# Kernel tuning notes

Hardware: AMD Instinct MI355X
Metric: run time of the kernel (lower is better)

## Reference

```python
import jax, jax.numpy as jnp
import numpy as np

TOP_K = 2

def setup_inputs() -> dict:
    key = jax.random.key(0)
    ks = jax.random.split(key, 5)
    B, S, H, F, E = 4, 512, 1024, 3584, 8
    x = jax.random.normal(ks[0], (B, S, H), dtype=jnp.float32)
    gate_w = jax.random.normal(ks[1], (H, E), dtype=jnp.float32) * (1.0 / np.sqrt(H))
    w1 = jax.random.normal(ks[2], (E, F, H), dtype=jnp.float32) * (1.0 / np.sqrt(H))
    w3 = jax.random.normal(ks[3], (E, F, H), dtype=jnp.float32) * (1.0 / np.sqrt(H))
    w2 = jax.random.normal(ks[4], (E, H, F), dtype=jnp.float32) * (1.0 / np.sqrt(F))
    return {"x": x, "gate_w": gate_w, "w1": w1, "w3": w3, "w2": w2}


def reference(x, gate_w, w1, w3, w2):
    # MoE top-2 routing (Mixtral-style), dense-dispatch formulation.
    B, S, H = x.shape
    E = gate_w.shape[1]
    xt = x.reshape(-1, H)                      # [T, H] flattened tokens
    T = xt.shape[0]
    logits = xt @ gate_w                       # [T, E] gate logits
    top_w, top_i = jax.lax.top_k(logits, TOP_K)    # [T, K]
    top_w = jax.nn.softmax(top_w, axis=-1)         # softmax over selected-k logits
    # combine[t, e] = routing weight of expert e for token t (0 if not selected)
    combine = jnp.zeros((T, E), dtype=xt.dtype)
    combine = combine.at[jnp.arange(T)[:, None], top_i].add(top_w)
    # SwiGLU experts: y_e = w2_e @ (silu(w1_e x) * (w3_e x))
    h = jnp.einsum('th,efh->tef', xt, w1)      # [T, E, F]
    g = jnp.einsum('th,efh->tef', xt, w3)      # [T, E, F]
    act = jax.nn.silu(h) * g                   # [T, E, F]
    out_e = jnp.einsum('tef,ehf->teh', act, w2)  # [T, E, H]
    out = jnp.einsum('teh,te->th', out_e, combine)  # weighted combine over experts
    return out.reshape(B, S, H)
```

## Files before the change

### kernel.cpp

```cpp
#include <hip/hip_runtime.h>
#include <hip/hip_bf16.h>
#include <stdint.h>

#define TOKENS 2048
#define HDIM 1024
#define FDIM 3584
#define NEXP 8
#define BK 32

typedef __attribute__((ext_vector_type(8))) short short8;
typedef __attribute__((ext_vector_type(4))) float floatx4;

#define AS1 __attribute__((address_space(1)))
#define AS3 __attribute__((address_space(3)))

__device__ __forceinline__ void glds16(const void* g, void* l) {
  __builtin_amdgcn_global_load_lds((const AS1 void*)g, (AS3 void*)l, 16, 0, 0);
}

__device__ __forceinline__ unsigned short f2bf(float f) {
  union { float f; unsigned int u; } c; c.f = f;
  unsigned int u = c.u;
  u += 0x7fffu + ((u >> 16) & 1u);
  return (unsigned short)(u >> 16);
}

__device__ __forceinline__ unsigned int pk2bf(float a, float b) {
  __hip_bfloat162 h = __float22bfloat162_rn(make_float2(a, b));
  union { __hip_bfloat162 h; unsigned int u; } c; c.h = h;
  return c.u;
}

__device__ __forceinline__ short8 pack_bf16(float4 c0, float4 c1) {
  union { short8 s; uint4 u; } o;
  o.u.x = pk2bf(c0.x, c0.y); o.u.y = pk2bf(c0.z, c0.w);
  o.u.z = pk2bf(c1.x, c1.y); o.u.w = pk2bf(c1.z, c1.w);
  return o.s;
}

__global__ void gate_kernel(const float* __restrict__ x,
                            const float* __restrict__ gw,
                            int* __restrict__ top_e,
                            float* __restrict__ top_w,
                            int* __restrict__ count) {
  int wv = threadIdx.x >> 6;
  int lane = threadIdx.x & 63;
  int t = blockIdx.x * 4 + wv;
  if (t >= TOKENS) return;
  float p[NEXP];
#pragma unroll
  for (int e = 0; e < NEXP; e++) p[e] = 0.f;
  const float* xr = x + (size_t)t * HDIM;
  for (int h = lane; h < HDIM; h += 64) {
    float xv = xr[h];
    const float4* g4 = (const float4*)(gw + (size_t)h * NEXP);
    float4 a = g4[0], b = g4[1];
    p[0] += xv * a.x; p[1] += xv * a.y; p[2] += xv * a.z; p[3] += xv * a.w;
    p[4] += xv * b.x; p[5] += xv * b.y; p[6] += xv * b.z; p[7] += xv * b.w;
  }
#pragma unroll
  for (int e = 0; e < NEXP; e++) {
#pragma unroll
    for (int off = 32; off > 0; off >>= 1) p[e] += __shfl_xor(p[e], off, 64);
  }
  if (lane == 0) {
    int i0 = 0;
    for (int e = 1; e < NEXP; e++) if (p[e] > p[i0]) i0 = e;
    int i1 = (i0 == 0) ? 1 : 0;
    for (int e = 0; e < NEXP; e++) if (e != i0 && p[e] > p[i1]) i1 = e;
    float l0 = p[i0], l1 = p[i1];
    float e1 = __expf(l1 - l0);
    float s = 1.f + e1;
    top_e[t * 2] = i0; top_e[t * 2 + 1] = i1;
    top_w[t * 2] = 1.f / s; top_w[t * 2 + 1] = e1 / s;
    atomicAdd(&count[i0], 1);
    atomicAdd(&count[i1], 1);
  }
}

__global__ void offsets_kernel(const int* __restrict__ count,
                               int* __restrict__ offs,
                               int* __restrict__ cursor) {
  if (threadIdx.x == 0 && blockIdx.x == 0) {
    int o = 0;
    for (int e = 0; e < NEXP; e++) { offs[e] = o; cursor[e] = o; o += count[e]; }
  }
}

__global__ void scatter_kernel(const int* __restrict__ top_e,
                               int* __restrict__ cursor,
                               int* __restrict__ tok_of,
                               int* __restrict__ slot_of) {
  int t = blockIdx.x * blockDim.x + threadIdx.x;
  if (t >= TOKENS) return;
#pragma unroll
  for (int k = 0; k < 2; k++) {
    int e = top_e[t * 2 + k];
    int g = atomicAdd(&cursor[e], 1);
    tok_of[g] = t;
    slot_of[t * 2 + k] = g;
  }
}

__global__ void xconv_kernel(const float* __restrict__ x,
                             unsigned short* __restrict__ xbf) {
  int i = (blockIdx.x * blockDim.x + threadIdx.x) * 4;
  float4 v = *(const float4*)(x + i);
  uint2 pk;
  pk.x = pk2bf(v.x, v.y);
  pk.y = pk2bf(v.z, v.w);
  *(uint2*)(xbf + i) = pk;
}

#define G1_BM 128
#define G1_BF 64

__global__ __launch_bounds__(256, 3)
void gemm1_kernel(const unsigned short* __restrict__ xbf,
                  const float* __restrict__ w1,
                  const float* __restrict__ w3,
                  const int* __restrict__ count,
                  const int* __restrict__ offs,
                  const int* __restrict__ tok_of,
                  unsigned short* __restrict__ act) {
  int e = blockIdx.z;
  int cnt = count[e];
  int m0 = blockIdx.y * G1_BM;
  if (m0 >= cnt) return;
  int f0 = blockIdx.x * G1_BF;
  int off_e = offs[e];

  __shared__ __align__(16) unsigned short sA[G1_BM * 32];
  __shared__ __align__(16) float sB1[G1_BF * 32];
  __shared__ __align__(16) float sB3[G1_BF * 32];

  int tid = threadIdx.x;
  int lane = tid & 63, wv = tid >> 6;

  const unsigned short* ag[2];
  char* alb[2];
  const float* g1p[2]; const float* g3p[2];
  char* blb[2];
#pragma unroll
  for (int p = 0; p < 2; p++) {
    int c = tid + p * 256;
    {
      int row = c >> 2, slot = c & 3;
      int gch = slot ^ ((row >> 1) & 3);
      int r = m0 + row;
      int tok = tok_of[off_e + (r < cnt ? r : 0)];
      ag[p] = xbf + (size_t)tok * HDIM + gch * 8;
      alb[p] = (char*)sA + (wv * 64 + p * 256) * 16;
    }
    {
      int row = c >> 3, slot = c & 7;
      int gch = slot ^ (row & 7);
      g1p[p] = w1 + ((size_t)e * FDIM + f0 + row) * HDIM + gch * 4;
      g3p[p] = w3 + ((size_t)e * FDIM + f0 + row) * HDIM + gch * 4;
      blb[p] = (char*)sB1 + (wv * 64 + p * 256) * 16;
    }
  }
  size_t b3delta = (char*)sB3 - (char*)sB1;

  int lrow = lane & 15, quad = lane >> 4;
  int wm = wv >> 1, wn = wv & 1;

  floatx4 acc1[4][2], acc3[4][2];
#pragma unroll
  for (int i = 0; i < 4; i++)
#pragma unroll
    for (int j = 0; j < 2; j++) {
      acc1[i][j] = (floatx4){0.f, 0.f, 0.f, 0.f};
      acc3[i][j] = (floatx4){0.f, 0.f, 0.f, 0.f};
    }

  for (int k0 = 0; k0 < HDIM; k0 += BK) {
    __syncthreads();
#pragma unroll
    for (int p = 0; p < 2; p++) {
      glds16(ag[p] + k0, alb[p]);
      glds16(g1p[p] + k0, blb[p]);
      glds16(g3p[p] + k0, blb[p] + b3delta);
    }
    __syncthreads();

    short8 af[4], b1f[2], b3f[2];
#pragma unroll
    for (int ms = 0; ms < 4; ms++) {
      int r = wm * 64 + ms * 16 + lrow;
      int sl = quad ^ ((r >> 1) & 3);
      af[ms] = *(const short8*)(sA + r * 32 + sl * 8);
    }
#pragma unroll
    for (int ns = 0; ns < 2; ns++) {
      int r = wn * 32 + ns * 16 + lrow;
      int s0 = (2 * quad) ^ (r & 7), s1 = (2 * quad + 1) ^ (r & 7);
      float4 c0 = *(const float4*)(sB1 + r * 32 + s0 * 4);
      float4 c1 = *(const float4*)(sB1 + r * 32 + s1 * 4);
      b1f[ns] = pack_bf16(c0, c1);
      float4 d0 = *(const float4*)(sB3 + r * 32 + s0 * 4);
      float4 d1 = *(const float4*)(sB3 + r * 32 + s1 * 4);
      b3f[ns] = pack_bf16(d0, d1);
    }
#pragma unroll
    for (int ms = 0; ms < 4; ms++)
#pragma unroll
      for (int ns = 0; ns < 2; ns++) {
        acc1[ms][ns] = __builtin_amdgcn_mfma_f32_16x16x32_bf16(af[ms], b1f[ns], acc1[ms][ns], 0, 0, 0);
        acc3[ms][ns] = __builtin_amdgcn_mfma_f32_16x16x32_bf16(af[ms], b3f[ns], acc3[ms][ns], 0, 0, 0);
      }
  }

#pragma unroll
  for (int ms = 0; ms < 4; ms++) {
#pragma unroll
    for (int reg = 0; reg < 4; reg++) {
      int slot = m0 + wm * 64 + ms * 16 + quad * 4 + reg;
      if (slot < cnt) {
        unsigned short* ar = act + (size_t)(off_e + slot) * FDIM + f0 + wn * 32;
#pragma unroll
        for (int ns = 0; ns < 2; ns++) {
          float h = acc1[ms][ns][reg];
          float g = acc3[ms][ns][reg];
          float a = h / (1.f + __expf(-h)) * g;
          ar[ns * 16 + lrow] = f2bf(a);
        }
      }
    }
  }
}

#define G2_BM 128
#define G2_BN 128
#define SPLITK 4
#define G2_KS (FDIM / SPLITK)

__global__ __launch_bounds__(256, 3)
void gemm2_kernel(const unsigned short* __restrict__ act,
                  const float* __restrict__ w2,
                  const int* __restrict__ count,
                  const int* __restrict__ offs,
                  float* __restrict__ part) {
  int zz = blockIdx.z;
  int e = zz & 7, sk = zz >> 3;
  int cnt = count[e];
  int m0 = blockIdx.y * G2_BM;
  if (m0 >= cnt) return;
  int h0 = blockIdx.x * G2_BN;
  int off_e = offs[e];
  int kb = sk * G2_KS;

  __shared__ __align__(16) unsigned short sA[G2_BM * 32];
  __shared__ __align__(16) float sB[G2_BN * 32];

  int tid = threadIdx.x;
  int lane = tid & 63, wv = tid >> 6;

  const unsigned short* ag[2];
  char* alb[2];
#pragma unroll
  for (int p = 0; p < 2; p++) {
    int c = tid + p * 256;
    int row = c >> 2, slot = c & 3;
    int gch = slot ^ ((row >> 1) & 3);
    int r = m0 + row;
    int rr = (r < cnt ? r : 0);
    ag[p] = act + (size_t)(off_e + rr) * FDIM + kb + gch * 8;
    alb[p] = (char*)sA + (wv * 64 + p * 256) * 16;
  }
  const float* bg[4];
  char* blb[4];
#pragma unroll
  for (int p = 0; p < 4; p++) {
    int c = tid + p * 256;
    int row = c >> 3, slot = c & 7;
    int gch = slot ^ (row & 7);
    bg[p] = w2 + ((size_t)e * HDIM + h0 + row) * FDIM + kb + gch * 4;
    blb[p] = (char*)sB + (wv * 64 + p * 256) * 16;
  }

  int lrow = lane & 15, quad = lane >> 4;
  int wm = wv >> 1, wn = wv & 1;

  floatx4 acc[4][4];
#pragma unroll
  for (int i = 0; i < 4; i++)
#pragma unroll
    for (int j = 0; j < 4; j++) acc[i][j] = (floatx4){0.f, 0.f, 0.f, 0.f};

  for (int k0 = 0; k0 < G2_KS; k0 += BK) {
    __syncthreads();
#pragma unroll
    for (int p = 0; p < 2; p++) glds16(ag[p] + k0, alb[p]);
#pragma unroll
    for (int p = 0; p < 4; p++) glds16(bg[p] + k0, blb[p]);
    __syncthreads();

    short8 af[4], bf[4];
#pragma unroll
    for (int ms = 0; ms < 4; ms++) {
      int r = wm * 64 + ms * 16 + lrow;
      int sl = quad ^ ((r >> 1) & 3);
      af[ms] = *(const short8*)(sA + r * 32 + sl * 8);
    }
#pragma unroll
    for (int ns = 0; ns < 4; ns++) {
      int r = wn * 64 + ns * 16 + lrow;
      int s0 = (2 * quad) ^ (r & 7), s1 = (2 * quad + 1) ^ (r & 7);
      float4 c0 = *(const float4*)(sB + r * 32 + s0 * 4);
      float4 c1 = *(const float4*)(sB + r * 32 + s1 * 4);
      bf[ns] = pack_bf16(c0, c1);
    }
#pragma unroll
    for (int ms = 0; ms < 4; ms++)
#pragma unroll
      for (int ns = 0; ns < 4; ns++)
        acc[ms][ns] = __builtin_amdgcn_mfma_f32_16x16x32_bf16(af[ms], bf[ns], acc[ms][ns], 0, 0, 0);
  }

#pragma unroll
  for (int ms = 0; ms < 4; ms++) {
#pragma unroll
    for (int reg = 0; reg < 4; reg++) {
      int slot = m0 + wm * 64 + ms * 16 + quad * 4 + reg;
      if (slot < cnt) {
        float* crow = part + ((size_t)sk * 4096 + off_e + slot) * HDIM + h0 + wn * 64;
#pragma unroll
        for (int ns = 0; ns < 4; ns++)
          crow[ns * 16 + lrow] = acc[ms][ns][reg];
      }
    }
  }
}

__global__ void combine_kernel(const float* __restrict__ part,
                               const int* __restrict__ slot_of,
                               const float* __restrict__ top_w,
                               float* __restrict__ out) {
  int t = blockIdx.x;
  int g0 = slot_of[t * 2], g1 = slot_of[t * 2 + 1];
  float w0 = top_w[t * 2], w1 = top_w[t * 2 + 1];
  int i = threadIdx.x;
  float4 s0 = {0.f, 0.f, 0.f, 0.f}, s1 = {0.f, 0.f, 0.f, 0.f};
#pragma unroll
  for (int sk = 0; sk < SPLITK; sk++) {
    float4 a = ((const float4*)(part + ((size_t)sk * 4096 + g0) * HDIM))[i];
    float4 b = ((const float4*)(part + ((size_t)sk * 4096 + g1) * HDIM))[i];
    s0.x += a.x; s0.y += a.y; s0.z += a.z; s0.w += a.w;
    s1.x += b.x; s1.y += b.y; s1.z += b.z; s1.w += b.w;
  }
  float4 r;
  r.x = w0 * s0.x + w1 * s1.x;
  r.y = w0 * s0.y + w1 * s1.y;
  r.z = w0 * s0.z + w1 * s1.z;
  r.w = w0 * s0.w + w1 * s1.w;
  ((float4*)(out + (size_t)t * HDIM))[i] = r;
}

extern "C" void kernel_launch(void* const* d_in, const int* in_sizes, int n_in,
                              void* d_out, int out_size, void* d_ws, size_t ws_size,
                              hipStream_t stream) {
  const float* x  = (const float*)d_in[0];
  const float* gw = (const float*)d_in[1];
  const float* w1 = (const float*)d_in[2];
  const float* w3 = (const float*)d_in[3];
  const float* w2 = (const float*)d_in[4];
  float* out = (float*)d_out;

  char* ws = (char*)d_ws;
  const size_t XBF_OFF = 0;
  const size_t ACT_OFF = 4ull << 20;
  const size_t PART_OFF = 36ull << 20;
  const size_t SML_OFF = 100ull << 20;

  unsigned short* xbf = (unsigned short*)(ws + XBF_OFF);
  unsigned short* act = (unsigned short*)(ws + ACT_OFF);
  float* part = (float*)(ws + PART_OFF);
  float* top_w = (float*)(ws + SML_OFF);
  int* top_e   = (int*)(ws + SML_OFF + 16384);
  int* slot_of = (int*)(ws + SML_OFF + 32768);
  int* tok_of  = (int*)(ws + SML_OFF + 49152);
  int* count   = (int*)(ws + SML_OFF + 65536);
  int* offs    = (int*)(ws + SML_OFF + 65536 + 32);
  int* cursor  = (int*)(ws + SML_OFF + 65536 + 64);

  hipMemsetAsync(count, 0, 96, stream);

  gate_kernel<<<TOKENS / 4, 256, 0, stream>>>(x, gw, top_e, top_w, count);
  offsets_kernel<<<1, 64, 0, stream>>>(count, offs, cursor);
  scatter_kernel<<<TOKENS / 256, 256, 0, stream>>>(top_e, cursor, tok_of, slot_of);
  xconv_kernel<<<(TOKENS * HDIM) / (256 * 4), 256, 0, stream>>>(x, xbf);
  gemm1_kernel<<<dim3(FDIM / G1_BF, TOKENS / G1_BM, NEXP), 256, 0, stream>>>(
      xbf, w1, w3, count, offs, tok_of, act);
  gemm2_kernel<<<dim3(HDIM / G2_BN, TOKENS / G2_BM, NEXP * SPLITK), 256, 0, stream>>>(
      act, w2, count, offs, part);
  combine_kernel<<<TOKENS, 256, 0, stream>>>(part, slot_of, top_w, out);
}
```

Before: 562.8 us.

## Pre-convert expert weights to bf16 and merge routing kernels into one

A new kernel converts w1, w3 and w2 from fp32 to bf16 in workspace on every call. Both GEMMs then stream bf16 weights straight into LDS, which halves weight bytes per tile and removes the per-iteration fp32→bf16 packing in the inner loop. This trades an extra full pass over the weights (fp32 read plus bf16 write) against the repeated fp32 weight traffic across M tiles. Separately, the histogram, offsets and scatter steps are fused into one single-block route kernel using shared-memory atomics, which removes the memset and two launches.

```diff
diff --git a/kernel.cpp b/kernel.cpp
--- a/kernel.cpp
+++ b/kernel.cpp
@@ -31,18 +31,10 @@
   return c.u;
 }
 
-__device__ __forceinline__ short8 pack_bf16(float4 c0, float4 c1) {
-  union { short8 s; uint4 u; } o;
-  o.u.x = pk2bf(c0.x, c0.y); o.u.y = pk2bf(c0.z, c0.w);
-  o.u.z = pk2bf(c1.x, c1.y); o.u.w = pk2bf(c1.z, c1.w);
-  return o.s;
-}
-
 __global__ void gate_kernel(const float* __restrict__ x,
                             const float* __restrict__ gw,
                             int* __restrict__ top_e,
-                            float* __restrict__ top_w,
-                            int* __restrict__ count) {
+                            float* __restrict__ top_w) {
   int wv = threadIdx.x >> 6;
   int lane = threadIdx.x & 63;
   int t = blockIdx.x * 4 + wv;
@@ -73,32 +65,40 @@
     float s = 1.f + e1;
     top_e[t * 2] = i0; top_e[t * 2 + 1] = i1;
     top_w[t * 2] = 1.f / s; top_w[t * 2 + 1] = e1 / s;
-    atomicAdd(&count[i0], 1);
-    atomicAdd(&count[i1], 1);
-  }
-}
-
-__global__ void offsets_kernel(const int* __restrict__ count,
-                               int* __restrict__ offs,
-                               int* __restrict__ cursor) {
-  if (threadIdx.x == 0 && blockIdx.x == 0) {
+  }
+}
+
+__global__ void route_kernel(const int* __restrict__ top_e,
+                             int* __restrict__ count,
+                             int* __restrict__ offs,
+                             int* __restrict__ tok_of,
+                             int* __restrict__ slot_of) {
+  __shared__ int hist[NEXP];
+  __shared__ int cur[NEXP];
+  int tid = threadIdx.x;
+  if (tid < NEXP) hist[tid] = 0;
+  __syncthreads();
+  int e[4];
+#pragma unroll
+  for (int j = 0; j < 4; j++) {
+    int i = tid * 4 + j;
+    e[j] = top_e[i];
+    atomicAdd(&hist[e[j]], 1);
+  }
+  __syncthreads();
+  if (tid == 0) {
     int o = 0;
-    for (int e = 0; e < NEXP; e++) { offs[e] = o; cursor[e] = o; o += count[e]; }
-  }
-}
-
-__global__ void scatter_kernel(const int* __restrict__ top_e,
-                               int* __restrict__ cursor,
-                               int* __restrict__ tok_of,
-                               int* __restrict__ slot_of) {
-  int t = blockIdx.x * blockDim.x + threadIdx.x;
-  if (t >= TOKENS) return;
-#pragma unroll
-  for (int k = 0; k < 2; k++) {
-    int e = top_e[t * 2 + k];
-    int g = atomicAdd(&cursor[e], 1);
-    tok_of[g] = t;
-    slot_of[t * 2 + k] = g;
+    for (int k = 0; k < NEXP; k++) {
+      offs[k] = o; cur[k] = o; count[k] = hist[k]; o += hist[k];
+    }
+  }
+  __syncthreads();
+#pragma unroll
+  for (int j = 0; j < 4; j++) {
+    int i = tid * 4 + j;
+    int g = atomicAdd(&cur[e[j]], 1);
+    tok_of[g] = i >> 1;
+    slot_of[i] = g;
   }
 }
 
@@ -112,13 +112,31 @@
   *(uint2*)(xbf + i) = pk;
 }
 
+__global__ void wconv_kernel(const float* __restrict__ w1,
+                             const float* __restrict__ w3,
+                             const float* __restrict__ w2,
+                             unsigned short* __restrict__ b1,
+                             unsigned short* __restrict__ b3,
+                             unsigned short* __restrict__ b2) {
+  int z = blockIdx.y;
+  const float* src = (z == 0) ? w1 : (z == 1) ? w3 : w2;
+  unsigned short* dst = (z == 0) ? b1 : (z == 1) ? b3 : b2;
+  size_t i = ((size_t)blockIdx.x * 256 + threadIdx.x) * 8;
+  float4 a = *(const float4*)(src + i);
+  float4 b = *(const float4*)(src + i + 4);
+  uint4 o;
+  o.x = pk2bf(a.x, a.y); o.y = pk2bf(a.z, a.w);
+  o.z = pk2bf(b.x, b.y); o.w = pk2bf(b.z, b.w);
+  *(uint4*)(dst + i) = o;
+}
+
 #define G1_BM 128
 #define G1_BF 64
 
 __global__ __launch_bounds__(256, 3)
 void gemm1_kernel(const unsigned short* __restrict__ xbf,
-                  const float* __restrict__ w1,
-                  const float* __restrict__ w3,
+                  const unsigned short* __restrict__ w1b,
+                  const unsigned short* __restrict__ w3b,
                   const int* __restrict__ count,
                   const int* __restrict__ offs,
                   const int* __restrict__ tok_of,
@@ -131,36 +149,35 @@
   int off_e = offs[e];
 
   __shared__ __align__(16) unsigned short sA[G1_BM * 32];
-  __shared__ __align__(16) float sB1[G1_BF * 32];
-  __shared__ __align__(16) float sB3[G1_BF * 32];
+  __shared__ __align__(16) unsigned short sB1[G1_BF * 32];
+  __shared__ __align__(16) unsigned short sB3[G1_BF * 32];
 
   int tid = threadIdx.x;
   int lane = tid & 63, wv = tid >> 6;
 
   const unsigned short* ag[2];
   char* alb[2];
-  const float* g1p[2]; const float* g3p[2];
-  char* blb[2];
 #pragma unroll
   for (int p = 0; p < 2; p++) {
     int c = tid + p * 256;
-    {
-      int row = c >> 2, slot = c & 3;
-      int gch = slot ^ ((row >> 1) & 3);
-      int r = m0 + row;
-      int tok = tok_of[off_e + (r < cnt ? r : 0)];
-      ag[p] = xbf + (size_t)tok * HDIM + gch * 8;
-      alb[p] = (char*)sA + (wv * 64 + p * 256) * 16;
-    }
-    {
-      int row = c >> 3, slot = c & 7;
-      int gch = slot ^ (row & 7);
-      g1p[p] = w1 + ((size_t)e * FDIM + f0 + row) * HDIM + gch * 4;
-      g3p[p] = w3 + ((size_t)e * FDIM + f0 + row) * HDIM + gch * 4;
-      blb[p] = (char*)sB1 + (wv * 64 + p * 256) * 16;
-    }
-  }
-  size_t b3delta = (char*)sB3 - (char*)sB1;
+    int row = c >> 2, slot = c & 3;
+    int gch = slot ^ ((row >> 1) & 3);
+    int r = m0 + row;
+    int tok = tok_of[off_e + (r < cnt ? r : 0)];
+    ag[p] = xbf + (size_t)tok * HDIM + gch * 8;
+    alb[p] = (char*)sA + (wv * 64 + p * 256) * 16;
+  }
+  const unsigned short *b1g, *b3g;
+  char *b1l, *b3l;
+  {
+    int row = tid >> 2, slot = tid & 3;
+    int gch = slot ^ ((row >> 1) & 3);
+    size_t wrow = (size_t)e * FDIM + f0 + row;
+    b1g = w1b + wrow * HDIM + gch * 8;
+    b3g = w3b + wrow * HDIM + gch * 8;
+    b1l = (char*)sB1 + (wv * 64) * 16;
+    b3l = (char*)sB3 + (wv * 64) * 16;
+  }
 
   int lrow = lane & 15, quad = lane >> 4;
   int wm = wv >> 1, wn = wv & 1;
@@ -177,11 +194,9 @@
   for (int k0 = 0; k0 < HDIM; k0 += BK) {
     __syncthreads();
 #pragma unroll
-    for (int p = 0; p < 2; p++) {
-      glds16(ag[p] + k0, alb[p]);
-      glds16(g1p[p] + k0, blb[p]);
-      glds16(g3p[p] + k0, blb[p] + b3delta);
-    }
+    for (int p = 0; p < 2; p++) glds16(ag[p] + k0, alb[p]);
+    glds16(b1g + k0, b1l);
+    glds16(b3g + k0, b3l);
     __syncthreads();
 
     short8 af[4], b1f[2], b3f[2];
@@ -194,13 +209,9 @@
 #pragma unroll
     for (int ns = 0; ns < 2; ns++) {
       int r = wn * 32 + ns * 16 + lrow;
-      int s0 = (2 * quad) ^ (r & 7), s1 = (2 * quad + 1) ^ (r & 7);
-      float4 c0 = *(const float4*)(sB1 + r * 32 + s0 * 4);
-      float4 c1 = *(const float4*)(sB1 + r * 32 + s1 * 4);
-      b1f[ns] = pack_bf16(c0, c1);
-      float4 d0 = *(const float4*)(sB3 + r * 32 + s0 * 4);
-      float4 d1 = *(const float4*)(sB3 + r * 32 + s1 * 4);
-      b3f[ns] = pack_bf16(d0, d1);
+      int sl = quad ^ ((r >> 1) & 3);
+      b1f[ns] = *(const short8*)(sB1 + r * 32 + sl * 8);
+      b3f[ns] = *(const short8*)(sB3 + r * 32 + sl * 8);
     }
 #pragma unroll
     for (int ms = 0; ms < 4; ms++)
@@ -237,7 +248,7 @@
 
 __global__ __launch_bounds__(256, 3)
 void gemm2_kernel(const unsigned short* __restrict__ act,
-                  const float* __restrict__ w2,
+                  const unsigned short* __restrict__ w2b,
                   const int* __restrict__ count,
                   const int* __restrict__ offs,
                   float* __restrict__ part) {
@@ -251,7 +262,7 @@
   int kb = sk * G2_KS;
 
   __shared__ __align__(16) unsigned short sA[G2_BM * 32];
-  __shared__ __align__(16) float sB[G2_BN * 32];
+  __shared__ __align__(16) unsigned short sB[G2_BN * 32];
 
   int tid = threadIdx.x;
   int lane = tid & 63, wv = tid >> 6;
@@ -268,14 +279,14 @@
     ag[p] = act + (size_t)(off_e + rr) * FDIM + kb + gch * 8;
     alb[p] = (char*)sA + (wv * 64 + p * 256) * 16;
   }
-  const float* bg[4];
-  char* blb[4];
-#pragma unroll
-  for (int p = 0; p < 4; p++) {
+  const unsigned short* bg[2];
+  char* blb[2];
+#pragma unroll
+  for (int p = 0; p < 2; p++) {
     int c = tid + p * 256;
-    int row = c >> 3, slot = c & 7;
-    int gch = slot ^ (row & 7);
-    bg[p] = w2 + ((size_t)e * HDIM + h0 + row) * FDIM + kb + gch * 4;
+    int row = c >> 2, slot = c & 3;
+    int gch = slot ^ ((row >> 1) & 3);
+    bg[p] = w2b + ((size_t)e * HDIM + h0 + row) * FDIM + kb + gch * 8;
     blb[p] = (char*)sB + (wv * 64 + p * 256) * 16;
   }
 
@@ -293,7 +304,7 @@
 #pragma unroll
     for (int p = 0; p < 2; p++) glds16(ag[p] + k0, alb[p]);
 #pragma unroll
-    for (int p = 0; p < 4; p++) glds16(bg[p] + k0, blb[p]);
+    for (int p = 0; p < 2; p++) glds16(bg[p] + k0, blb[p]);
     __syncthreads();
 
     short8 af[4], bf[4];
@@ -306,10 +317,8 @@
 #pragma unroll
     for (int ns = 0; ns < 4; ns++) {
       int r = wn * 64 + ns * 16 + lrow;
-      int s0 = (2 * quad) ^ (r & 7), s1 = (2 * quad + 1) ^ (r & 7);
-      float4 c0 = *(const float4*)(sB + r * 32 + s0 * 4);
-      float4 c1 = *(const float4*)(sB + r * 32 + s1 * 4);
-      bf[ns] = pack_bf16(c0, c1);
+      int sl = quad ^ ((r >> 1) & 3);
+      bf[ns] = *(const short8*)(sB + r * 32 + sl * 8);
     }
 #pragma unroll
     for (int ms = 0; ms < 4; ms++)
@@ -368,31 +377,28 @@
   float* out = (float*)d_out;
 
   char* ws = (char*)d_ws;
-  const size_t XBF_OFF = 0;
-  const size_t ACT_OFF = 4ull << 20;
-  const size_t PART_OFF = 36ull << 20;
-  const size_t SML_OFF = 100ull << 20;
-
-  unsigned short* xbf = (unsigned short*)(ws + XBF_OFF);
-  unsigned short* act = (unsigned short*)(ws + ACT_OFF);
-  float* part = (float*)(ws + PART_OFF);
-  float* top_w = (float*)(ws + SML_OFF);
-  int* top_e   = (int*)(ws + SML_OFF + 16384);
-  int* slot_of = (int*)(ws + SML_OFF + 32768);
-  int* tok_of  = (int*)(ws + SML_OFF + 49152);
-  int* count   = (int*)(ws + SML_OFF + 65536);
-  int* offs    = (int*)(ws + SML_OFF + 65536 + 32);
-  int* cursor  = (int*)(ws + SML_OFF + 65536 + 64);
-
-  hipMemsetAsync(count, 0, 96, stream);
-
-  gate_kernel<<<TOKENS / 4, 256, 0, stream>>>(x, gw, top_e, top_w, count);
-  offsets_kernel<<<1, 64, 0, stream>>>(count, offs, cursor);
-  scatter_kernel<<<TOKENS / 256, 256, 0, stream>>>(top_e, cursor, tok_of, slot_of);
+  const size_t MB = 1ull << 20;
+  float* top_w = (float*)(ws);
+  int* top_e   = (int*)(ws + 16384);
+  int* slot_of = (int*)(ws + 32768);
+  int* tok_of  = (int*)(ws + 49152);
+  int* count   = (int*)(ws + 65536);
+  int* offs    = (int*)(ws + 65536 + 64);
+
+  unsigned short* xbf = (unsigned short*)(ws + 1 * MB);
+  unsigned short* act = (unsigned short*)(ws + 5 * MB);
+  unsigned short* w2b = (unsigned short*)(ws + 35 * MB);
+  unsigned short* w1b = (unsigned short*)(ws + 94 * MB);
+  unsigned short* w3b = (unsigned short*)(ws + 150 * MB);
+  float* part = (float*)(ws + 94 * MB);
+
+  gate_kernel<<<TOKENS / 4, 256, 0, stream>>>(x, gw, top_e, top_w);
+  route_kernel<<<1, 1024, 0, stream>>>(top_e, count, offs, tok_of, slot_of);
   xconv_kernel<<<(TOKENS * HDIM) / (256 * 4), 256, 0, stream>>>(x, xbf);
+  wconv_kernel<<<dim3(14336, 3), 256, 0, stream>>>(w1, w3, w2, w1b, w3b, w2b);
   gemm1_kernel<<<dim3(FDIM / G1_BF, TOKENS / G1_BM, NEXP), 256, 0, stream>>>(
-      xbf, w1, w3, count, offs, tok_of, act);
+      xbf, w1b, w3b, count, offs, tok_of, act);
   gemm2_kernel<<<dim3(HDIM / G2_BN, TOKENS / G2_BM, NEXP * SPLITK), 256, 0, stream>>>(
-      act, w2, count, offs, part);
+      act, w2b, count, offs, part);
   combine_kernel<<<TOKENS, 256, 0, stream>>>(part, slot_of, top_w, out);
 }
```

Result: faster. 528.9 us (-6.0%).
